# Optimization experiments

Measured on AMD Instinct MI355X. Metric: run time of the kernel, lower is better.

Reference implementation:

```python
import jax, jax.numpy as jnp
import numpy as np

N = 8192   # instances in bag
L = 384    # feature dim (dino_bloom_small -> self.L = 384)
D = 128    # attention hidden dim (self.D)
C = 5      # class_count


def setup_inputs() -> dict:
    key = jax.random.key(0)
    ks = jax.random.split(key, 9)
    s = 0.05
    return {
        "x": jax.random.normal(ks[0], (N, L), dtype=jnp.float32),
        # attention_multi_column: Linear(L,D) -> Tanh -> Linear(D,C)
        "aW1": jax.random.normal(ks[1], (L, D), dtype=jnp.float32) * s,
        "ab1": jax.random.normal(ks[2], (D,), dtype=jnp.float32) * s,
        "aW2": jax.random.normal(ks[3], (D, C), dtype=jnp.float32) * s,
        "ab2": jax.random.normal(ks[4], (C,), dtype=jnp.float32) * s,
        # per-class classifiers: Linear(L,64) -> ReLU -> Linear(64,1), batched over C
        "cW1": jax.random.normal(ks[5], (C, L, 64), dtype=jnp.float32) * s,
        "cb1": jax.random.normal(ks[6], (C, 64), dtype=jnp.float32) * s,
        "cW2": jax.random.normal(ks[7], (C, 64), dtype=jnp.float32) * s,
        "cb2": jax.random.normal(ks[8], (C,), dtype=jnp.float32) * s,
    }


def _pairwise_euclidean(ft):
    # ||a-b|| via Gram expansion; avoids the O(N^2*L) broadcast intermediate
    sq = jnp.sum(ft * ft, axis=1)                      # [N]
    d2 = sq[:, None] + sq[None, :] - 2.0 * (ft @ ft.T)  # [N,N]
    d2 = jnp.maximum(d2, 0.0)
    # safe sqrt (zero on diagonal, matches torch.norm subgradient convention)
    return jnp.where(d2 > 0.0, jnp.sqrt(jnp.where(d2 > 0.0, d2, 1.0)), 0.0)


def reference(x, aW1, ab1, aW2, ab2, cW1, cb1, cW2, cb2):
    ft = x  # encoder is identity for dino_bloom_small
    dist = _pairwise_euclidean(ft)                      # [N,N]
    # multicolumn attention: logits per class, softmax over instances
    att = jnp.tanh(ft @ aW1 + ab1) @ aW2 + ab2          # [N,C]
    att_sm = jax.nn.softmax(att, axis=0)                # softmax over N per class
    bag = att_sm.T @ ft                                 # [C,L] bag features per class
    # per-class classifier heads, batched over class dim
    h = jax.nn.relu(jnp.einsum('cl,clh->ch', bag, cW1) + cb1)  # [C,64]
    pred = jnp.sum(h * cW2, axis=1) + cb2               # [C]
    return pred[None, :], dist
```

## Files before the change

kernel.cpp:

```cpp
#include <hip/hip_runtime.h>
#include <cstdint>
#include <cstddef>

#define N_INST 8192
#define L_DIM  384
#define D_DIM  128
#define C_CLS  5

typedef __bf16 bf16x8 __attribute__((ext_vector_type(8)));
typedef float  f32x4  __attribute__((ext_vector_type(4)));
typedef float  f32x4u __attribute__((ext_vector_type(4), aligned(4)));

typedef __attribute__((address_space(1))) void gvoid_t;
typedef __attribute__((address_space(3))) void lvoid_t;

__device__ __forceinline__ unsigned short f2bf(float f) {
  unsigned u = __float_as_uint(f);
  unsigned r = (u + 0x7FFFu + ((u >> 16) & 1u)) >> 16;
  return (unsigned short)r;
}
__device__ __forceinline__ float bf2f(unsigned short b) {
  return __uint_as_float(((unsigned)b) << 16);
}

__device__ __forceinline__ void gload_lds16(const void* g, void* lds) {
  __builtin_amdgcn_global_load_lds(
      (gvoid_t*)(uintptr_t)g,
      (lvoid_t*)(uint32_t)(uintptr_t)lds,
      16, 0, 0);
}

__global__ __launch_bounds__(256) void prep_x_kernel(
    const float* __restrict__ x, unsigned short* __restrict__ xbf,
    float* __restrict__ sq) {
  int w = threadIdx.x >> 6, lane = threadIdx.x & 63;
  int row = blockIdx.x * 4 + w;
  const float* xr = x + (size_t)row * L_DIM;
  unsigned short* br = xbf + (size_t)row * L_DIM;
  float s = 0.f;
#pragma unroll
  for (int k = 0; k < 6; ++k) {
    float v = xr[lane + 64 * k];
    unsigned short b = f2bf(v);
    br[lane + 64 * k] = b;
    float vb = bf2f(b);
    s = fmaf(vb, vb, s);
  }
#pragma unroll
  for (int off = 32; off; off >>= 1) s += __shfl_down(s, off, 64);
  if (lane == 0) sq[row] = s;
}

__global__ __launch_bounds__(256) void prep_w_kernel(
    const float* __restrict__ aW1, unsigned short* __restrict__ w1t) {
  int idx = blockIdx.x * 256 + threadIdx.x;
  int d = idx / L_DIM, l = idx - d * L_DIM;
  w1t[idx] = f2bf(aW1[(size_t)l * D_DIM + d]);
}

template <int MODE>
__global__ __launch_bounds__(256, 2) void gemm_kernel(
    const unsigned short* __restrict__ amat,
    const unsigned short* __restrict__ bmat,
    const float* __restrict__ sqv,
    const float* __restrict__ bias,
    float* __restrict__ out) {
  __shared__ alignas(16) unsigned short As[128][64];
  __shared__ alignas(16) unsigned short Bs[128][64];

  int tid = threadIdx.x;
  int w = tid >> 6, lane = tid & 63;
  int wr = w >> 1, wc = w & 1;

  int ti, tj;
  if (MODE == 0) { ti = blockIdx.x >> 6; tj = blockIdx.x & 63; }
  else           { ti = blockIdx.x;      tj = 0; }
  int i0 = ti * 128, j0 = tj * 128;

  const unsigned short* asrc = amat + (size_t)i0 * L_DIM;
  const unsigned short* bsrc = bmat + (size_t)j0 * L_DIM;

  f32x4 acc[4][4];
#pragma unroll
  for (int m = 0; m < 4; ++m)
#pragma unroll
    for (int n = 0; n < 4; ++n) acc[m][n] = (f32x4){0.f, 0.f, 0.f, 0.f};

  int lrow = lane & 15, lkb = lane >> 4;

  for (int kc = 0; kc < 6; ++kc) {
    int k0 = kc * 64;
#pragma unroll
    for (int c = 0; c < 4; ++c) {
      int rb = c * 32 + w * 8;
      const unsigned short* ga =
          asrc + (size_t)(rb + (lane >> 3)) * L_DIM + k0 + (lane & 7) * 8;
      gload_lds16(ga, &As[rb][0]);
      const unsigned short* gb =
          bsrc + (size_t)(rb + (lane >> 3)) * L_DIM + k0 + (lane & 7) * 8;
      gload_lds16(gb, &Bs[rb][0]);
    }
    __syncthreads();
#pragma unroll
    for (int kk = 0; kk < 64; kk += 32) {
      bf16x8 af[4], bfr[4];
#pragma unroll
      for (int m = 0; m < 4; ++m)
        af[m] = *(const bf16x8*)&As[wr * 64 + m * 16 + lrow][kk + lkb * 8];
#pragma unroll
      for (int n = 0; n < 4; ++n)
        bfr[n] = *(const bf16x8*)&Bs[wc * 64 + n * 16 + lrow][kk + lkb * 8];
#pragma unroll
      for (int m = 0; m < 4; ++m)
#pragma unroll
        for (int n = 0; n < 4; ++n)
          acc[m][n] = __builtin_amdgcn_mfma_f32_16x16x32_bf16(
              bfr[n], af[m], acc[m][n], 0, 0, 0);
    }
    __syncthreads();
  }

  if (MODE == 0) {
#pragma unroll
    for (int m = 0; m < 4; ++m) {
      int gi = i0 + wr * 64 + m * 16 + lrow;
      float si = sqv[gi];
      float* orow = out + (size_t)gi * N_INST;
#pragma unroll
      for (int n = 0; n < 4; ++n) {
        int gjb = j0 + wc * 64 + n * 16 + lkb * 4;
        f32x4 sj = *(const f32x4*)&sqv[gjb];
        f32x4u o;
#pragma unroll
        for (int r = 0; r < 4; ++r) {
          float d2 = si + sj[r] - 2.f * acc[m][n][r];
          float dv = (d2 > 0.f) ? sqrtf(d2) : 0.f;
          if (gi == gjb + r) dv = 0.f;
          o[r] = dv;
        }
        *(f32x4u*)&orow[gjb] = o;
      }
    }
  } else {
#pragma unroll
    for (int m = 0; m < 4; ++m) {
      int gi = i0 + wr * 64 + m * 16 + lrow;
      float* orow = out + (size_t)gi * D_DIM;
#pragma unroll
      for (int n = 0; n < 4; ++n) {
        int d0 = wc * 64 + n * 16 + lkb * 4;
        f32x4 bv = *(const f32x4*)&bias[d0];
        f32x4 o;
#pragma unroll
        for (int r = 0; r < 4; ++r) o[r] = tanhf(acc[m][n][r] + bv[r]);
        *(f32x4*)&orow[d0] = o;
      }
    }
  }
}

__global__ __launch_bounds__(256) void attc_kernel(
    const float* __restrict__ h, const float* __restrict__ aW2,
    const float* __restrict__ ab2, float* __restrict__ exp_att,
    float* __restrict__ colsum) {
  __shared__ float csum[C_CLS];
  if (threadIdx.x < C_CLS) csum[threadIdx.x] = 0.f;
  __syncthreads();
  int i = blockIdx.x * 256 + threadIdx.x;
  float a[C_CLS];
#pragma unroll
  for (int c = 0; c < C_CLS; ++c) a[c] = ab2[c];
  const float* hr = h + (size_t)i * D_DIM;
  for (int d = 0; d < D_DIM; ++d) {
    float hv = hr[d];
#pragma unroll
    for (int c = 0; c < C_CLS; ++c) a[c] = fmaf(hv, aW2[d * C_CLS + c], a[c]);
  }
#pragma unroll
  for (int c = 0; c < C_CLS; ++c) {
    float e = expf(a[c]);
    exp_att[(size_t)i * C_CLS + c] = e;
    atomicAdd(&csum[c], e);
  }
  __syncthreads();
  if (threadIdx.x < C_CLS) atomicAdd(&colsum[threadIdx.x], csum[threadIdx.x]);
}

__global__ __launch_bounds__(256) void bag_kernel(
    const float* __restrict__ x, const float* __restrict__ exp_att,
    float* __restrict__ bagU) {
  int t = threadIdx.x;
  int rbase = blockIdx.x * 32;
  float acc0[C_CLS] = {0, 0, 0, 0, 0}, acc1[C_CLS] = {0, 0, 0, 0, 0};
  int l0 = t, l1 = t + 256;
  for (int i = rbase; i < rbase + 32; ++i) {
    const float* xr = x + (size_t)i * L_DIM;
    float e[C_CLS];
#pragma unroll
    for (int c = 0; c < C_CLS; ++c) e[c] = exp_att[(size_t)i * C_CLS + c];
    float x0 = xr[l0];
#pragma unroll
    for (int c = 0; c < C_CLS; ++c) acc0[c] = fmaf(e[c], x0, acc0[c]);
    if (t < 128) {
      float x1 = xr[l1];
#pragma unroll
      for (int c = 0; c < C_CLS; ++c) acc1[c] = fmaf(e[c], x1, acc1[c]);
    }
  }
#pragma unroll
  for (int c = 0; c < C_CLS; ++c) atomicAdd(&bagU[c * L_DIM + l0], acc0[c]);
  if (t < 128)
#pragma unroll
    for (int c = 0; c < C_CLS; ++c) atomicAdd(&bagU[c * L_DIM + l1], acc1[c]);
}

__global__ __launch_bounds__(256) void final_kernel(
    const float* __restrict__ bagU, const float* __restrict__ colsum,
    const float* __restrict__ cW1, const float* __restrict__ cb1,
    const float* __restrict__ cW2, const float* __restrict__ cb2,
    float* __restrict__ out) {
  __shared__ float bag_s[C_CLS * L_DIM];
  __shared__ float h_s[C_CLS * 64];
  int t = threadIdx.x;
  for (int idx = t; idx < C_CLS * L_DIM; idx += 256) {
    int c = idx / L_DIM;
    bag_s[idx] = bagU[idx] / colsum[c];
  }
  __syncthreads();
  for (int idx = t; idx < C_CLS * 64; idx += 256) {
    int c = idx >> 6, hh = idx & 63;
    float acc = cb1[idx];
    for (int l = 0; l < L_DIM; ++l)
      acc = fmaf(bag_s[c * L_DIM + l], cW1[(size_t)(c * L_DIM + l) * 64 + hh], acc);
    h_s[idx] = fmaxf(acc, 0.f) * cW2[idx];
  }
  __syncthreads();
  if (t < C_CLS) {
    float p = cb2[t];
    for (int hh = 0; hh < 64; ++hh) p += h_s[t * 64 + hh];
    out[t] = p;
  }
}

extern "C" void kernel_launch(void* const* d_in, const int* in_sizes, int n_in,
                              void* d_out, int out_size, void* d_ws,
                              size_t ws_size, hipStream_t stream) {
  const float* x   = (const float*)d_in[0];
  const float* aW1 = (const float*)d_in[1];
  const float* ab1 = (const float*)d_in[2];
  const float* aW2 = (const float*)d_in[3];
  const float* ab2 = (const float*)d_in[4];
  const float* cW1 = (const float*)d_in[5];
  const float* cb1 = (const float*)d_in[6];
  const float* cW2 = (const float*)d_in[7];
  const float* cb2 = (const float*)d_in[8];
  float* outp = (float*)d_out;

  char* ws = (char*)d_ws;
  unsigned short* xbf = (unsigned short*)(ws);
  unsigned short* w1t = (unsigned short*)(ws + 6291456);
  float* sq           = (float*)(ws + 6389760);
  float* h_tanh       = (float*)(ws + 6422528);
  float* exp_att      = (float*)(ws + 10616832);
  float* colsum       = (float*)(ws + 10780672);
  float* bagU         = (float*)(ws + 10780736);

  hipMemsetAsync(ws + 10780672, 0, 64 + C_CLS * L_DIM * 4, stream);

  prep_x_kernel<<<2048, 256, 0, stream>>>(x, xbf, sq);
  prep_w_kernel<<<192, 256, 0, stream>>>(aW1, w1t);
  gemm_kernel<1><<<64, 256, 0, stream>>>(xbf, w1t, nullptr, ab1, h_tanh);
  attc_kernel<<<32, 256, 0, stream>>>(h_tanh, aW2, ab2, exp_att, colsum);
  bag_kernel<<<256, 256, 0, stream>>>(x, exp_att, bagU);
  final_kernel<<<1, 256, 0, stream>>>(bagU, colsum, cW1, cb1, cW2, cb2, outp);
  gemm_kernel<0><<<4096, 256, 0, stream>>>(xbf, xbf, sq, nullptr, outp + C_CLS);
}
```

Measured before the change: 192.8 us.

## Exploit distance matrix symmetry with upper-triangular tiles and LDS-staged coalesced stores

The pairwise distance GEMM now launches only the upper-triangular 128x128 tiles (2080 instead of 4096). Each off-diagonal tile writes both its own block and its transpose, which roughly halves the MFMA and operand-load work. The output is staged through a padded LDS buffer so each row is written with aligned 16-byte vector stores, working around the 5-float offset of the output buffer. The cost is extra LDS traffic, more barriers, a larger shared-memory footprint that may reduce occupancy, and scattered transposed writes; the kernel stays bound by its 256MB output write.

```diff
diff --git a/kernel.cpp b/kernel.cpp
--- a/kernel.cpp
+++ b/kernel.cpp
@@ -9,7 +9,6 @@
 
 typedef __bf16 bf16x8 __attribute__((ext_vector_type(8)));
 typedef float  f32x4  __attribute__((ext_vector_type(4)));
-typedef float  f32x4u __attribute__((ext_vector_type(4), aligned(4)));
 
 typedef __attribute__((address_space(1))) void gvoid_t;
 typedef __attribute__((address_space(3))) void lvoid_t;
@@ -58,11 +57,9 @@
   w1t[idx] = f2bf(aW1[(size_t)l * D_DIM + d]);
 }
 
-template <int MODE>
-__global__ __launch_bounds__(256, 2) void gemm_kernel(
+__global__ __launch_bounds__(256, 2) void attn_gemm_kernel(
     const unsigned short* __restrict__ amat,
     const unsigned short* __restrict__ bmat,
-    const float* __restrict__ sqv,
     const float* __restrict__ bias,
     float* __restrict__ out) {
   __shared__ alignas(16) unsigned short As[128][64];
@@ -71,14 +68,10 @@
   int tid = threadIdx.x;
   int w = tid >> 6, lane = tid & 63;
   int wr = w >> 1, wc = w & 1;
-
-  int ti, tj;
-  if (MODE == 0) { ti = blockIdx.x >> 6; tj = blockIdx.x & 63; }
-  else           { ti = blockIdx.x;      tj = 0; }
-  int i0 = ti * 128, j0 = tj * 128;
+  int i0 = blockIdx.x * 128;
 
   const unsigned short* asrc = amat + (size_t)i0 * L_DIM;
-  const unsigned short* bsrc = bmat + (size_t)j0 * L_DIM;
+  const unsigned short* bsrc = bmat;
 
   f32x4 acc[4][4];
 #pragma unroll
@@ -93,12 +86,10 @@
 #pragma unroll
     for (int c = 0; c < 4; ++c) {
       int rb = c * 32 + w * 8;
-      const unsigned short* ga =
-          asrc + (size_t)(rb + (lane >> 3)) * L_DIM + k0 + (lane & 7) * 8;
-      gload_lds16(ga, &As[rb][0]);
-      const unsigned short* gb =
-          bsrc + (size_t)(rb + (lane >> 3)) * L_DIM + k0 + (lane & 7) * 8;
-      gload_lds16(gb, &Bs[rb][0]);
+      gload_lds16(asrc + (size_t)(rb + (lane >> 3)) * L_DIM + k0 + (lane & 7) * 8,
+                  &As[rb][0]);
+      gload_lds16(bsrc + (size_t)(rb + (lane >> 3)) * L_DIM + k0 + (lane & 7) * 8,
+                  &Bs[rb][0]);
     }
     __syncthreads();
 #pragma unroll
@@ -119,42 +110,164 @@
     }
     __syncthreads();
   }
-
-  if (MODE == 0) {
-#pragma unroll
-    for (int m = 0; m < 4; ++m) {
+#pragma unroll
+  for (int m = 0; m < 4; ++m) {
+    int gi = i0 + wr * 64 + m * 16 + lrow;
+    float* orow = out + (size_t)gi * D_DIM;
+#pragma unroll
+    for (int n = 0; n < 4; ++n) {
+      int d0 = wc * 64 + n * 16 + lkb * 4;
+      f32x4 bv = *(const f32x4*)&bias[d0];
+      f32x4 o;
+#pragma unroll
+      for (int r = 0; r < 4; ++r) o[r] = tanhf(acc[m][n][r] + bv[r]);
+      *(f32x4*)&orow[d0] = o;
+    }
+  }
+}
+
+__global__ __launch_bounds__(256, 2) void dist_kernel(
+    const unsigned short* __restrict__ xbf, const float* __restrict__ sqv,
+    float* __restrict__ F) {
+  __shared__ alignas(16) unsigned short As[128][64];
+  __shared__ alignas(16) unsigned short Bs[128][64];
+  __shared__ alignas(16) float T[64][132];
+
+  int b = blockIdx.x;
+  int ti = (int)((129.0 - sqrt(129.0 * 129.0 - 8.0 * (double)b)) * 0.5);
+  while ((ti + 1) * (129 - (ti + 1)) / 2 <= b) ++ti;
+  while (ti * (129 - ti) / 2 > b) --ti;
+  int tj = ti + (b - ti * (129 - ti) / 2);
+  int i0 = ti * 128, j0 = tj * 128;
+
+  int tid = threadIdx.x;
+  int w = tid >> 6, lane = tid & 63;
+  int wr = w >> 1, wc = w & 1;
+  int lrow = lane & 15, lkb = lane >> 4;
+
+  const unsigned short* asrc = xbf + (size_t)i0 * L_DIM;
+  const unsigned short* bsrc = xbf + (size_t)j0 * L_DIM;
+
+  f32x4 acc[4][4];
+#pragma unroll
+  for (int m = 0; m < 4; ++m)
+#pragma unroll
+    for (int n = 0; n < 4; ++n) acc[m][n] = (f32x4){0.f, 0.f, 0.f, 0.f};
+
+  for (int kc = 0; kc < 6; ++kc) {
+    int k0 = kc * 64;
+#pragma unroll
+    for (int c = 0; c < 4; ++c) {
+      int rb = c * 32 + w * 8;
+      gload_lds16(asrc + (size_t)(rb + (lane >> 3)) * L_DIM + k0 + (lane & 7) * 8,
+                  &As[rb][0]);
+      gload_lds16(bsrc + (size_t)(rb + (lane >> 3)) * L_DIM + k0 + (lane & 7) * 8,
+                  &Bs[rb][0]);
+    }
+    __syncthreads();
+#pragma unroll
+    for (int kk = 0; kk < 64; kk += 32) {
+      bf16x8 af[4], bfr[4];
+#pragma unroll
+      for (int m = 0; m < 4; ++m)
+        af[m] = *(const bf16x8*)&As[wr * 64 + m * 16 + lrow][kk + lkb * 8];
+#pragma unroll
+      for (int n = 0; n < 4; ++n)
+        bfr[n] = *(const bf16x8*)&Bs[wc * 64 + n * 16 + lrow][kk + lkb * 8];
+#pragma unroll
+      for (int m = 0; m < 4; ++m)
+#pragma unroll
+        for (int n = 0; n < 4; ++n)
+          acc[m][n] = __builtin_amdgcn_mfma_f32_16x16x32_bf16(
+              bfr[n], af[m], acc[m][n], 0, 0, 0);
+    }
+    __syncthreads();
+  }
+
+  int rgrp = tid >> 5, k = tid & 31;
+
+#pragma unroll
+  for (int chunk = 0; chunk < 2; ++chunk) {
+#pragma unroll
+    for (int mlo = 0; mlo < 2; ++mlo) {
+      int m = chunk * 2 + mlo;
       int gi = i0 + wr * 64 + m * 16 + lrow;
       float si = sqv[gi];
-      float* orow = out + (size_t)gi * N_INST;
+      int t = wr * 32 + mlo * 16 + lrow;
 #pragma unroll
       for (int n = 0; n < 4; ++n) {
-        int gjb = j0 + wc * 64 + n * 16 + lkb * 4;
-        f32x4 sj = *(const f32x4*)&sqv[gjb];
-        f32x4u o;
+        int jl = wc * 64 + n * 16 + lkb * 4;
+        f32x4 sj = *(const f32x4*)&sqv[j0 + jl];
+        f32x4 o;
 #pragma unroll
         for (int r = 0; r < 4; ++r) {
           float d2 = si + sj[r] - 2.f * acc[m][n][r];
           float dv = (d2 > 0.f) ? sqrtf(d2) : 0.f;
-          if (gi == gjb + r) dv = 0.f;
+          if (gi == j0 + jl + r) dv = 0.f;
           o[r] = dv;
         }
-        *(f32x4u*)&orow[gjb] = o;
+        *(f32x4*)&T[t][jl] = o;
       }
     }
-  } else {
-#pragma unroll
-    for (int m = 0; m < 4; ++m) {
-      int gi = i0 + wr * 64 + m * 16 + lrow;
-      float* orow = out + (size_t)gi * D_DIM;
-#pragma unroll
-      for (int n = 0; n < 4; ++n) {
-        int d0 = wc * 64 + n * 16 + lkb * 4;
-        f32x4 bv = *(const f32x4*)&bias[d0];
-        f32x4 o;
-#pragma unroll
-        for (int r = 0; r < 4; ++r) o[r] = tanhf(acc[m][n][r] + bv[r]);
-        *(f32x4*)&orow[d0] = o;
+    __syncthreads();
+#pragma unroll
+    for (int it = 0; it < 8; ++it) {
+      int t = it * 8 + rgrp;
+      int gi = i0 + (t >> 5) * 64 + chunk * 32 + (t & 31);
+      float* row = F + 5 + (size_t)gi * N_INST + j0;
+      if (k < 31) {
+        int jj = 3 + 4 * k;
+        f32x4 v;
+        v[0] = T[t][jj]; v[1] = T[t][jj + 1];
+        v[2] = T[t][jj + 2]; v[3] = T[t][jj + 3];
+        *(f32x4*)&row[jj] = v;
+      } else {
+        row[0] = T[t][0]; row[1] = T[t][1]; row[2] = T[t][2];
+        row[127] = T[t][127];
       }
+    }
+    __syncthreads();
+  }
+
+  if (ti != tj) {
+#pragma unroll
+    for (int cn = 0; cn < 2; ++cn) {
+#pragma unroll
+      for (int nlo = 0; nlo < 2; ++nlo) {
+        int n = cn * 2 + nlo;
+        int jl = wc * 64 + n * 16 + lkb * 4;
+        f32x4 sj = *(const f32x4*)&sqv[j0 + jl];
+        int u0 = wc * 32 + nlo * 16 + lkb * 4;
+#pragma unroll
+        for (int m = 0; m < 4; ++m) {
+          int il = wr * 64 + m * 16 + lrow;
+          float si = sqv[i0 + il];
+#pragma unroll
+          for (int r = 0; r < 4; ++r) {
+            float d2 = si + sj[r] - 2.f * acc[m][n][r];
+            float dv = (d2 > 0.f) ? sqrtf(d2) : 0.f;
+            T[u0 + r][il] = dv;
+          }
+        }
+      }
+      __syncthreads();
+#pragma unroll
+      for (int it = 0; it < 8; ++it) {
+        int u = it * 8 + rgrp;
+        int gj = j0 + (u >> 5) * 64 + cn * 32 + (u & 31);
+        float* row = F + 5 + (size_t)gj * N_INST + i0;
+        if (k < 31) {
+          int jj = 3 + 4 * k;
+          f32x4 v;
+          v[0] = T[u][jj]; v[1] = T[u][jj + 1];
+          v[2] = T[u][jj + 2]; v[3] = T[u][jj + 3];
+          *(f32x4*)&row[jj] = v;
+        } else {
+          row[0] = T[u][0]; row[1] = T[u][1]; row[2] = T[u][2];
+          row[127] = T[u][127];
+        }
+      }
+      __syncthreads();
     }
   }
 }
@@ -269,9 +382,9 @@
 
   prep_x_kernel<<<2048, 256, 0, stream>>>(x, xbf, sq);
   prep_w_kernel<<<192, 256, 0, stream>>>(aW1, w1t);
-  gemm_kernel<1><<<64, 256, 0, stream>>>(xbf, w1t, nullptr, ab1, h_tanh);
+  attn_gemm_kernel<<<64, 256, 0, stream>>>(xbf, w1t, ab1, h_tanh);
   attc_kernel<<<32, 256, 0, stream>>>(h_tanh, aW2, ab2, exp_att, colsum);
   bag_kernel<<<256, 256, 0, stream>>>(x, exp_att, bagU);
   final_kernel<<<1, 256, 0, stream>>>(bagU, colsum, cW1, cb1, cW2, cb2, outp);
-  gemm_kernel<0><<<4096, 256, 0, stream>>>(xbf, xbf, sq, nullptr, outp + C_CLS);
-}
+  dist_kernel<<<2080, 256, 0, stream>>>(xbf, sq, outp);
+}
```

Measured after the change: 217.1 us. +12.6%, slower.
